# Performance work log

Hardware: AMD Instinct MI355X
Metric: run time of the kernel (lower is better)

Reference implementation:

```python
import jax, jax.numpy as jnp
import numpy as np

# Standard VVC 8-tap luma interpolation filter (16 fractional phases), /256 as in source
_LUMA = np.array([
    [0, 0, 0, 64, 0, 0, 0, 0],
    [0, 1, -3, 63, 4, -2, 1, 0],
    [-1, 2, -5, 62, 8, -3, 1, 0],
    [-1, 3, -8, 60, 13, -4, 1, 0],
    [-1, 4, -10, 58, 17, -5, 1, 0],
    [-1, 4, -11, 52, 26, -8, 3, -1],
    [-1, 3, -9, 47, 31, -10, 4, -1],
    [-1, 4, -11, 45, 34, -10, 4, -1],
    [-1, 4, -11, 40, 40, -11, 4, -1],
    [-1, 4, -10, 34, 45, -11, 4, -1],
    [-1, 4, -10, 31, 47, -9, 3, -1],
    [-1, 3, -8, 26, 52, -11, 4, -1],
    [0, 1, -5, 17, 58, -10, 4, -1],
    [0, 1, -4, 13, 60, -8, 3, -1],
    [0, 1, -3, 8, 62, -5, 2, -1],
    [0, 1, -2, 4, 63, -3, 1, 0]], dtype=np.float32) / 256.0

TAPS = 8          # filter_length for standard luma
LOG2_NORM = 12    # final normalization 2**12


def _phase_tables(out_len, in_len, scale):
    """Static (trace-time) per-output-position tap indices and fractional phase,
    replicating the source exactly: ref = int(i*16384/scale); integer = ref>>4; frac = ref&15;
    tap index = clamp(integer + k - TAPS//2 + 1, 0, in_len-1)."""
    refs = np.array([int(i * 16384 / scale) for i in range(out_len)], dtype=np.int64)
    integer = refs >> 4
    frac = refs & 15
    idx = np.clip(integer[:, None] + np.arange(TAPS)[None, :] - TAPS // 2 + 1, 0, in_len - 1)
    return jnp.asarray(idx, jnp.int32), jnp.asarray(frac, jnp.int32)


def _upsample(x, filt, scale):
    B, C, H, W = x.shape
    new_W, new_H = int(W * scale), int(H * scale)

    # Horizontal pass: per-output-column phase-dependent 8-tap MAC
    idx_w, frac_w = _phase_tables(new_W, W, scale)
    coef_w = filt[frac_w]                      # [new_W, TAPS]
    x_h = jnp.zeros((B, C, H, new_W), x.dtype)
    for k in range(TAPS):                      # small fixed tap loop, vectorized over B,C,H,new_W
        x_h = x_h + coef_w[:, k] * x[:, :, :, idx_w[:, k]]

    # Vertical pass: per-output-row phase-dependent 8-tap MAC
    idx_h, frac_h = _phase_tables(new_H, H, scale)
    coef_h = filt[frac_h]                      # [new_H, TAPS]
    x_v = jnp.zeros((B, C, new_H, new_W), x.dtype)
    for k in range(TAPS):
        x_v = x_v + coef_h[:, k][:, None] * x_h[:, :, idx_h[:, k], :]

    return x_v / (2 ** LOG2_NORM)


def setup_inputs() -> dict:
    key = jax.random.key(0)
    x = jax.random.normal(key, (2, 8, 540, 960), dtype=jnp.float32)
    return {"x": x, "luma_filter": jnp.asarray(_LUMA), "scale_factor": 3}


def reference(x, luma_filter, scale_factor):
    return _upsample(x, luma_filter, scale_factor)
```

## Files before the change

### kernel.cpp

```cpp
#include <hip/hip_runtime.h>

#define BC 16
#define H 540
#define W 960
#define OH 1620
#define OW 2880
#define NOUT (16u * 1620u * 2880u)

__global__ __launch_bounds__(256) void vtm_upsample(
    const float* __restrict__ x,
    const float* __restrict__ filt,
    const int* __restrict__ scale_p,
    float* __restrict__ out)
{
    __shared__ float s_f[16][8];
    __shared__ float s_sum[16];
    const int tid = threadIdx.x;
    if (tid < 128) ((float*)s_f)[tid] = filt[tid];
    __syncthreads();
    if (tid < 16) {
        float s = 0.f;
        #pragma unroll
        for (int k = 0; k < 8; ++k) s += s_f[tid][k];
        s_sum[tid] = s;
    }
    __syncthreads();

    const unsigned scale = (unsigned)scale_p[0];
    const float inv = 1.0f / 4096.0f;
    const unsigned nvec = NOUT / 4u;
    const unsigned stride = gridDim.x * blockDim.x;

    for (unsigned v = blockIdx.x * blockDim.x + (unsigned)tid; v < nvec; v += stride) {
        const unsigned p = v * 4u;
        const unsigned ox0 = p % OW;
        const unsigned rr  = p / OW;
        const unsigned oy  = rr % OH;
        const unsigned bc  = rr / OH;
        const float* __restrict__ xp = x + (size_t)bc * (H * W);

        const unsigned refy = (oy * 16384u) / scale;
        const int iy = (int)(refy >> 4);
        const int fy = (int)(refy & 15u);
        const int r0 = min(max(iy - 3, 0), H - 1);
        const int r7 = min(max(iy + 4, 0), H - 1);
        const bool rowSat = (r0 == r7);
        const float Sh = s_sum[fy];

        float vals[4];
        #pragma unroll
        for (int u = 0; u < 4; ++u) {
            const unsigned ox = ox0 + (unsigned)u;
            const unsigned refx = (ox * 16384u) / scale;
            const int ix = (int)(refx >> 4);
            const int fx = (int)(refx & 15u);
            const int c0 = min(max(ix - 3, 0), W - 1);
            const int c7 = min(max(ix + 4, 0), W - 1);
            const bool colSat = (c0 == c7);
            const float Sw = s_sum[fx];

            float val;
            if (colSat && rowSat) {
                val = xp[r0 * W + c0] * Sw * Sh;
            } else if (colSat) {
                float acc = 0.f;
                #pragma unroll
                for (int j = 0; j < 8; ++j) {
                    const int ry = min(max(iy + j - 3, 0), H - 1);
                    acc = fmaf(s_f[fy][j], xp[ry * W + c0], acc);
                }
                val = acc * Sw;
            } else if (rowSat) {
                float acc = 0.f;
                #pragma unroll
                for (int k = 0; k < 8; ++k) {
                    const int cx = min(max(ix + k - 3, 0), W - 1);
                    acc = fmaf(s_f[fx][k], xp[r0 * W + cx], acc);
                }
                val = acc * Sh;
            } else {
                float acc = 0.f;
                #pragma unroll
                for (int j = 0; j < 8; ++j) {
                    const int ry = min(max(iy + j - 3, 0), H - 1);
                    const float* __restrict__ rp = xp + ry * W;
                    float h = 0.f;
                    #pragma unroll
                    for (int k = 0; k < 8; ++k) {
                        const int cx = min(max(ix + k - 3, 0), W - 1);
                        h = fmaf(s_f[fx][k], rp[cx], h);
                    }
                    acc = fmaf(s_f[fy][j], h, acc);
                }
                val = acc;
            }
            vals[u] = val * inv;
        }
        float4 res = make_float4(vals[0], vals[1], vals[2], vals[3]);
        *reinterpret_cast<float4*>(out + p) = res;
    }
}

extern "C" void kernel_launch(void* const* d_in, const int* in_sizes, int n_in,
                              void* d_out, int out_size, void* d_ws, size_t ws_size,
                              hipStream_t stream) {
    const float* x      = (const float*)d_in[0];
    const float* filt   = (const float*)d_in[1];
    const int*   scale_p= (const int*)d_in[2];
    float* out = (float*)d_out;
    dim3 grid(4096), block(256);
    vtm_upsample<<<grid, block, 0, stream>>>(x, filt, scale_p, out);
}
```

Before: 357.4 us.

## Precompute row/column tap tables in shared memory and map channel to grid y

```diff
diff --git a/kernel.cpp b/kernel.cpp
--- a/kernel.cpp
+++ b/kernel.cpp
@@ -1,11 +1,11 @@
 #include <hip/hip_runtime.h>
 
-#define BC 16
-#define H 540
-#define W 960
-#define OH 1620
-#define OW 2880
-#define NOUT (16u * 1620u * 2880u)
+#define Hh 540
+#define Ww 960
+#define OHh 1620
+#define OWw 2880
+#define OW4 720
+#define PERC (OHh * OW4)
 
 __global__ __launch_bounds__(256) void vtm_upsample(
     const float* __restrict__ x,
@@ -15,7 +15,12 @@
 {
     __shared__ float s_f[16][8];
     __shared__ float s_sum[16];
+    __shared__ unsigned short rtab[OHh];
+    __shared__ uint2 ctab[OW4];
+
     const int tid = threadIdx.x;
+    const unsigned scale = (unsigned)*scale_p;
+
     if (tid < 128) ((float*)s_f)[tid] = filt[tid];
     __syncthreads();
     if (tid < 16) {
@@ -24,90 +29,99 @@
         for (int k = 0; k < 8; ++k) s += s_f[tid][k];
         s_sum[tid] = s;
     }
+    for (int i = tid; i < OHh; i += 256) {
+        const unsigned ref = ((unsigned)i * 16384u) / scale;
+        const int ii = (int)(ref >> 4);
+        const unsigned f = ref & 15u;
+        const int lo = min(max(ii - 3, 0), Hh - 1);
+        const int hi = min(max(ii + 4, 0), Hh - 1);
+        rtab[i] = (unsigned short)((unsigned)lo | (f << 10) | ((lo == hi) ? 0x4000u : 0u));
+    }
+    for (int g = tid; g < OW4; g += 256) {
+        unsigned e[4];
+        #pragma unroll
+        for (int u = 0; u < 4; ++u) {
+            const unsigned ox = (unsigned)(4 * g + u);
+            const unsigned ref = (ox * 16384u) / scale;
+            const int ii = (int)(ref >> 4);
+            const unsigned f = ref & 15u;
+            const int lo = min(max(ii - 3, 0), Ww - 1);
+            const int hi = min(max(ii + 4, 0), Ww - 1);
+            e[u] = (unsigned)lo | (f << 10) | ((lo == hi) ? 0x4000u : 0u);
+        }
+        ctab[g] = make_uint2(e[0] | (e[1] << 15), e[2] | (e[3] << 15));
+    }
     __syncthreads();
 
-    const unsigned scale = (unsigned)scale_p[0];
+    const unsigned bc = blockIdx.y;
+    const float* __restrict__ xp = x + (size_t)bc * (Hh * Ww);
+    float* __restrict__ op = out + (size_t)bc * ((size_t)OHh * OWw);
     const float inv = 1.0f / 4096.0f;
-    const unsigned nvec = NOUT / 4u;
-    const unsigned stride = gridDim.x * blockDim.x;
+    const unsigned stride = gridDim.x * 256u;
 
-    for (unsigned v = blockIdx.x * blockDim.x + (unsigned)tid; v < nvec; v += stride) {
-        const unsigned p = v * 4u;
-        const unsigned ox0 = p % OW;
-        const unsigned rr  = p / OW;
-        const unsigned oy  = rr % OH;
-        const unsigned bc  = rr / OH;
-        const float* __restrict__ xp = x + (size_t)bc * (H * W);
+    for (unsigned v = blockIdx.x * 256u + (unsigned)tid; v < PERC; v += stride) {
+        const unsigned g  = v % OW4;
+        const unsigned oy = v / OW4;
+        const unsigned rinfo = rtab[oy];
+        const uint2 ci = ctab[g];
+        const unsigned e0 = ci.x & 0x7FFFu, e1 = ci.x >> 15;
+        const unsigned e2 = ci.y & 0x7FFFu, e3 = ci.y >> 15;
+        const int r0 = (int)(rinfo & 1023u);
+        const float Sh = s_sum[(rinfo >> 10) & 15u];
+        float vals[4];
 
-        const unsigned refy = (oy * 16384u) / scale;
-        const int iy = (int)(refy >> 4);
-        const int fy = (int)(refy & 15u);
-        const int r0 = min(max(iy - 3, 0), H - 1);
-        const int r7 = min(max(iy + 4, 0), H - 1);
-        const bool rowSat = (r0 == r7);
-        const float Sh = s_sum[fy];
-
-        float vals[4];
-        #pragma unroll
-        for (int u = 0; u < 4; ++u) {
-            const unsigned ox = ox0 + (unsigned)u;
-            const unsigned refx = (ox * 16384u) / scale;
-            const int ix = (int)(refx >> 4);
-            const int fx = (int)(refx & 15u);
-            const int c0 = min(max(ix - 3, 0), W - 1);
-            const int c7 = min(max(ix + 4, 0), W - 1);
-            const bool colSat = (c0 == c7);
-            const float Sw = s_sum[fx];
-
-            float val;
-            if (colSat && rowSat) {
-                val = xp[r0 * W + c0] * Sw * Sh;
-            } else if (colSat) {
-                float acc = 0.f;
-                #pragma unroll
-                for (int j = 0; j < 8; ++j) {
-                    const int ry = min(max(iy + j - 3, 0), H - 1);
-                    acc = fmaf(s_f[fy][j], xp[ry * W + c0], acc);
+        if (rinfo & e0 & e1 & e2 & e3 & 0x4000u) {
+            const float c = Sh * inv;
+            const float* __restrict__ rp = xp + r0 * Ww;
+            vals[0] = rp[e0 & 1023u] * s_sum[(e0 >> 10) & 15u] * c;
+            vals[1] = rp[e1 & 1023u] * s_sum[(e1 >> 10) & 15u] * c;
+            vals[2] = rp[e2 & 1023u] * s_sum[(e2 >> 10) & 15u] * c;
+            vals[3] = rp[e3 & 1023u] * s_sum[(e3 >> 10) & 15u] * c;
+        } else {
+            const unsigned refy = ((unsigned)oy * 16384u) / scale;
+            const int iy = (int)(refy >> 4);
+            const int fy = (int)(refy & 15u);
+            const bool rsat = (rinfo & 0x4000u) != 0;
+            const unsigned ee[4] = {e0, e1, e2, e3};
+            #pragma unroll
+            for (int u = 0; u < 4; ++u) {
+                const unsigned e = ee[u];
+                if ((e & 0x4000u) && rsat) {
+                    vals[u] = xp[r0 * Ww + (int)(e & 1023u)] * s_sum[(e >> 10) & 15u] * Sh * inv;
+                } else {
+                    const unsigned ox = g * 4u + (unsigned)u;
+                    const unsigned refx = (ox * 16384u) / scale;
+                    const int ix = (int)(refx >> 4);
+                    const int fx = (int)(refx & 15u);
+                    float acc = 0.f;
+                    #pragma unroll
+                    for (int j = 0; j < 8; ++j) {
+                        const int ry = min(max(iy + j - 3, 0), Hh - 1);
+                        const float* __restrict__ rp2 = xp + ry * Ww;
+                        float h = 0.f;
+                        #pragma unroll
+                        for (int k = 0; k < 8; ++k) {
+                            const int cx = min(max(ix + k - 3, 0), Ww - 1);
+                            h = fmaf(s_f[fx][k], rp2[cx], h);
+                        }
+                        acc = fmaf(s_f[fy][j], h, acc);
+                    }
+                    vals[u] = acc * inv;
                 }
-                val = acc * Sw;
-            } else if (rowSat) {
-                float acc = 0.f;
-                #pragma unroll
-                for (int k = 0; k < 8; ++k) {
-                    const int cx = min(max(ix + k - 3, 0), W - 1);
-                    acc = fmaf(s_f[fx][k], xp[r0 * W + cx], acc);
-                }
-                val = acc * Sh;
-            } else {
-                float acc = 0.f;
-                #pragma unroll
-                for (int j = 0; j < 8; ++j) {
-                    const int ry = min(max(iy + j - 3, 0), H - 1);
-                    const float* __restrict__ rp = xp + ry * W;
-                    float h = 0.f;
-                    #pragma unroll
-                    for (int k = 0; k < 8; ++k) {
-                        const int cx = min(max(ix + k - 3, 0), W - 1);
-                        h = fmaf(s_f[fx][k], rp[cx], h);
-                    }
-                    acc = fmaf(s_f[fy][j], h, acc);
-                }
-                val = acc;
             }
-            vals[u] = val * inv;
         }
-        float4 res = make_float4(vals[0], vals[1], vals[2], vals[3]);
-        *reinterpret_cast<float4*>(out + p) = res;
+        *reinterpret_cast<float4*>(op + (size_t)oy * OWw + g * 4u) =
+            make_float4(vals[0], vals[1], vals[2], vals[3]);
     }
 }
 
 extern "C" void kernel_launch(void* const* d_in, const int* in_sizes, int n_in,
                               void* d_out, int out_size, void* d_ws, size_t ws_size,
                               hipStream_t stream) {
-    const float* x      = (const float*)d_in[0];
-    const float* filt   = (const float*)d_in[1];
-    const int*   scale_p= (const int*)d_in[2];
+    const float* x       = (const float*)d_in[0];
+    const float* filt    = (const float*)d_in[1];
+    const int*   scale_p = (const int*)d_in[2];
     float* out = (float*)d_out;
-    dim3 grid(4096), block(256);
+    dim3 grid(128, 16), block(256);
     vtm_upsample<<<grid, block, 0, stream>>>(x, filt, scale_p, out);
 }
```

Measured after the change: 421.5 us. 17.9% more time.
